# Performance work log

Measured on AMD Instinct MI355X. Metric: run time of the kernel, lower is better.

## Reference

```python
import jax, jax.numpy as jnp
import numpy as np
from jax import lax

# --- COSMO-SAC constants (defaults from the layer) ---
T = 623.15
Q0 = 79.53
R0 = 66.69
C_HB = 85580.0
RGAS = 8.3144598 / 4184.0
SIG_HB = 0.0084
EPS = 3.667
AEFF = 7.5
EO = 0.0002395
ZC = 10.0
X0 = 0.235
X1 = 1.0 - 0.235
N_SIGMA = 51
N_ITERS = 50


def _deltaw():
    s = np.linspace(-0.025, 0.025, N_SIGMA)
    sigma_m = np.tile(s, (N_SIGMA, 1))          # rows of grid values
    sigma_n = sigma_m.T
    sigma_acc = np.tril(sigma_n) + np.triu(sigma_m, 1)
    sigma_don = np.tril(sigma_m) + np.triu(sigma_n, 1)
    fpol = (EPS - 1.0) / (EPS + 0.5)
    alpha = 0.3 * AEFF ** 1.5 / EO
    alpha_prime = fpol * alpha
    dw = (alpha_prime / 2.0 * (sigma_m + sigma_n) ** 2
          + C_HB * np.maximum(0.0, sigma_acc - SIG_HB) * np.minimum(0.0, sigma_don + SIG_HB))
    return jnp.asarray(dw, jnp.float32)

DELTAW = _deltaw()                       # [51,51]
SSS = jnp.exp(-DELTAW / (RGAS * T))      # [51,51]


def get_Gamma(psigma):
    """50-step fixed-point solve. psigma: [B,51] -> Gamma: [B,51]."""
    AA = SSS[None, :, :] * psigma[:, None, :]   # [B,51,51]
    def step(G, _):
        Gnew = 1.0 / jnp.einsum('bmn,bn->bm', AA, G)
        return (Gnew + G) * 0.5, None
    G, _ = lax.scan(step, jnp.ones_like(psigma), None, length=N_ITERS)
    return G


def setup_inputs() -> dict:
    key = jax.random.key(0)
    k1, k2, k3, k4 = jax.random.split(key, 4)
    B = 32768
    return {
        "input_my_sigma": jax.random.uniform(k1, (B, N_SIGMA), dtype=jnp.float32),
        "v_compound": jax.random.uniform(k2, (B,), dtype=jnp.float32),
        "input_vt_sigma": jax.random.uniform(k3, (B, N_SIGMA, 2), dtype=jnp.float32),
        "v_vt": jax.random.uniform(k4, (B,), dtype=jnp.float32),
    }


def reference(input_my_sigma, v_compound, input_vt_sigma, v_vt):
    my = input_my_sigma                 # [B,51]
    vt = input_vt_sigma[:, :, 1]        # [B,51]
    A0 = jnp.sum(my, axis=1)            # [B]
    A1 = jnp.sum(vt, axis=1)            # [B]

    psigma_mix = (X0 * my + X1 * vt) / (X0 * A0[:, None] + X1 * A1[:, None])
    lnGamma_mix = jnp.log(get_Gamma(psigma_mix))       # [B,51]

    # residual part for component i = 0
    psigma = my / A0[:, None]
    lnGammai = jnp.log(get_Gamma(psigma))              # [B,51]
    lng_resid = A0 / AEFF * jnp.sum(psigma * (lnGamma_mix - lnGammai), axis=1)

    # combinatorial part (Staverman-Guggenheim)
    q0 = A0 / Q0
    q1 = A1 / Q0
    r0 = v_compound / R0
    r1 = v_vt / R0
    xq = X0 * q0 + X1 * q1
    xr = X0 * r0 + X1 * r1
    theta = X0 * q0 / xq
    phi = X0 * r0 / xr
    l0 = ZC / 2.0 * (r0 - q0) - (r0 - 1.0)
    l1 = ZC / 2.0 * (r1 - q1) - (r1 - 1.0)
    xl = X0 * l0 + X1 * l1
    lng_comb = (jnp.log(phi / X0) + ZC / 2.0 * q0 * jnp.log(theta / phi)
                + l0 - phi / X0 * xl)

    return (lng_resid + lng_comb)[:, None]             # [B,1]
```

## Files before the change

kernel.cpp:

```cpp
#include <hip/hip_runtime.h>

typedef __bf16 bf16;
typedef __attribute__((ext_vector_type(4))) bf16 bf16x4;
typedef __attribute__((ext_vector_type(8))) bf16 bf16x8;
typedef __attribute__((ext_vector_type(4))) float f32x4;

namespace {

constexpr double csqrt(double x) {
  double s = x > 1 ? x : 1;
  for (int i = 0; i < 60; ++i) s = 0.5 * (s + x / s);
  return s;
}
constexpr double AP_D =
    ((3.667 - 1.0) / (3.667 + 0.5)) * (0.3 * (7.5 * csqrt(7.5)) / 0.0002395);
constexpr double RGAST_D = (8.3144598 / 4184.0) * 623.15;

__device__ __forceinline__ float sss_val(int i, int j) {
  if (i > 50 || j > 50) return 0.0f;
  const float si = -0.025f + 0.001f * (float)i;
  const float sj = -0.025f + 0.001f * (float)j;
  const float acc = fmaxf(0.0f, fmaxf(si, sj) - 0.0084f);
  const float don = fminf(0.0f, fminf(si, sj) + 0.0084f);
  const float dw = (float)(AP_D * 0.5) * (si + sj) * (si + sj) + 85580.0f * acc * don;
  return expf(-dw * (float)(1.0 / RGAST_D));
}

__device__ __forceinline__ float fast_log(float x) {
  return __builtin_amdgcn_logf(x) * 0.69314718056f;
}

__device__ __forceinline__ f32x4 mfma16(bf16x8 a, bf16x8 b, f32x4 c) {
  return __builtin_amdgcn_mfma_f32_16x16x32_bf16(a, b, c, 0, 0, 0);
}

}

__global__ __launch_bounds__(64, 4) void cosmo_mfma_gt(
    const float* __restrict__ my_sigma,
    const float* __restrict__ v_comp,
    const float* __restrict__ vt_sigma,
    const float* __restrict__ v_vt,
    float* __restrict__ out,
    int B)
{
  __shared__ bf16 lds[16 * 68];

  const int lane = threadIdx.x;
  const int s    = lane & 15;
  const int g    = lane >> 4;
  const int e    = blockIdx.x * 8 + (s >> 1);
  const int task = s & 1;
  const bool ein = (e < B);
  const int  ec  = ein ? e : 0;

  float A0, A1, wC[16];
  {
    float myv[16], vtv[16];
#pragma unroll
    for (int t = 0; t < 4; ++t)
#pragma unroll
      for (int r = 0; r < 4; ++r) {
        const int n  = 16 * t + 4 * g + r;
        const bool nv = (n < 51) && ein;
        const int nc = (n < 51) ? n : 50;
        myv[4 * t + r] = nv ? my_sigma[(size_t)ec * 51 + nc] : 0.0f;
        vtv[4 * t + r] = nv ? vt_sigma[((size_t)ec * 51 + nc) * 2 + 1] : 0.0f;
      }
    float pA0 = 0.f, pA1 = 0.f;
#pragma unroll
    for (int i = 0; i < 16; ++i) { pA0 += myv[i]; pA1 += vtv[i]; }
    A0 = pA0; A0 += __shfl_xor(A0, 16, 64); A0 += __shfl_xor(A0, 32, 64);
    A1 = pA1; A1 += __shfl_xor(A1, 16, 64); A1 += __shfl_xor(A1, 32, 64);

    const float den  = task ? (0.235f * A0 + 0.765f * A1) : A0;
    const float rden = __builtin_amdgcn_rcpf(den);
#pragma unroll
    for (int i = 0; i < 16; ++i) {
      const float num = task ? (0.235f * myv[i] + 0.765f * vtv[i]) : myv[i];
      wC[i] = num * rden;
    }
  }

  float Gt[16];
#pragma unroll
  for (int i = 0; i < 16; ++i) Gt[i] = wC[i];

  bf16x8 afr[4][2];
#pragma unroll
  for (int t = 0; t < 4; ++t)
#pragma unroll
    for (int kt = 0; kt < 2; ++kt) {
      bf16x8 v;
#pragma unroll
      for (int i = 0; i < 8; ++i)
        v[i] = (bf16)sss_val(16 * t + s, 32 * kt + 8 * g + i);
      afr[t][kt] = v;
    }

  const int wb = s * 68 + 4 * g;
  const int rb = s * 68 + 8 * g;
  float padd[4];
#pragma unroll
  for (int r = 0; r < 4; ++r) padd[r] = (4 * g + r >= 3) ? 1.0f : 0.0f;

#pragma unroll 1
  for (int it = 0; it < 50; ++it) {
#pragma unroll
    for (int t = 0; t < 4; ++t) {
      bf16x4 hv;
#pragma unroll
      for (int r = 0; r < 4; ++r) hv[r] = (bf16)Gt[4 * t + r];
      *(bf16x4*)(lds + wb + 16 * t) = hv;
    }

    bf16x8 bfr[2];
#pragma unroll
    for (int kt = 0; kt < 2; ++kt) {
      const bf16x4 lo = *(const bf16x4*)(lds + rb + 32 * kt);
      const bf16x4 hi = *(const bf16x4*)(lds + rb + 32 * kt + 4);
      bfr[kt] = __builtin_shufflevector(lo, hi, 0, 1, 2, 3, 4, 5, 6, 7);
    }

    const f32x4 z = {};
    f32x4 acc[4];
#pragma unroll
    for (int t = 0; t < 4; ++t) acc[t] = mfma16(afr[t][0], bfr[0], z);
#pragma unroll
    for (int t = 0; t < 4; ++t) acc[t] = mfma16(afr[t][1], bfr[1], acc[t]);

#pragma unroll
    for (int t = 0; t < 3; ++t)
#pragma unroll
      for (int r = 0; r < 4; ++r) {
        const int i = 4 * t + r;
        const float rc = __builtin_amdgcn_rcpf(acc[t][r]);
        Gt[i] = 0.5f * __builtin_fmaf(wC[i], rc, Gt[i]);
      }
#pragma unroll
    for (int r = 0; r < 4; ++r) {
      const int i = 12 + r;
      const float rc = __builtin_amdgcn_rcpf(acc[3][r] + padd[r]);
      Gt[i] = 0.5f * __builtin_fmaf(wC[i], rc, Gt[i]);
    }
  }

  const float rA0 = __builtin_amdgcn_rcpf(A0);
  float Sp = 0.f;
#pragma unroll
  for (int t = 0; t < 4; ++t)
#pragma unroll
    for (int r = 0; r < 4; ++r) {
      const int n = 16 * t + 4 * g + r;
      if (n < 51) {
        const int i = 4 * t + r;
        const float p  = (ein ? my_sigma[(size_t)ec * 51 + n] : 0.0f) * rA0;
        const float gg = Gt[i] * __builtin_amdgcn_rcpf(wC[i]);
        Sp += p * __builtin_amdgcn_logf(gg);
      }
    }
  Sp += __shfl_xor(Sp, 16, 64);
  Sp += __shfl_xor(Sp, 32, 64);
  const float St = Sp * 0.69314718056f;
  const float So = __shfl_xor(St, 1, 64);

  if (task == 0 && g == 0 && ein) {
    const float lng_resid = A0 * (1.0f / 7.5f) * (So - St);
    const float v0  = v_comp[e];
    const float v1v = v_vt[e];
    const float q0 = A0 * (1.0f / 79.53f), q1 = A1 * (1.0f / 79.53f);
    const float r0 = v0 * (1.0f / 66.69f), r1 = v1v * (1.0f / 66.69f);
    const float xq = 0.235f * q0 + 0.765f * q1;
    const float xr = 0.235f * r0 + 0.765f * r1;
    const float theta = 0.235f * q0 * __builtin_amdgcn_rcpf(xq);
    const float phi   = 0.235f * r0 * __builtin_amdgcn_rcpf(xr);
    const float l0 = 5.0f * (r0 - q0) - (r0 - 1.0f);
    const float l1 = 5.0f * (r1 - q1) - (r1 - 1.0f);
    const float xl = 0.235f * l0 + 0.765f * l1;
    const float lng_comb = fast_log(phi * (1.0f / 0.235f))
                         + 5.0f * q0 * fast_log(theta * __builtin_amdgcn_rcpf(phi))
                         + l0 - (phi * (1.0f / 0.235f)) * xl;
    out[e] = lng_resid + lng_comb;
  }
}

extern "C" void kernel_launch(void* const* d_in, const int* in_sizes, int n_in,
                              void* d_out, int out_size, void* d_ws, size_t ws_size,
                              hipStream_t stream) {
  const float* my  = (const float*)d_in[0];
  const float* vc  = (const float*)d_in[1];
  const float* vts = (const float*)d_in[2];
  const float* vvt = (const float*)d_in[3];
  float* out = (float*)d_out;
  const int B = in_sizes[1];
  const int grid = (B + 7) / 8;
  cosmo_mfma_gt<<<grid, 64, 0, stream>>>(my, vc, vts, vvt, out, B);
}
```

Baseline: 122.6 us.

## Permute SSS K-ordering to feed MFMA B operand from registers, drop LDS

The SSS A-fragment columns are reordered so the K index each lane contributes matches the accumulator rows it already holds. The updated Gamma values can then go straight from registers into the B operand, with no per-iteration LDS write/read round trip. Blocks also grow from one to four wavefronts, each handling eight batch elements, so fewer blocks are launched. A guard against zero wC is added in the final log, which avoids a divide-by-zero on padded entries.

```diff
diff --git a/kernel.cpp b/kernel.cpp
--- a/kernel.cpp
+++ b/kernel.cpp
@@ -36,7 +36,7 @@
 
 }
 
-__global__ __launch_bounds__(64, 4) void cosmo_mfma_gt(
+__global__ __launch_bounds__(256, 4) void cosmo_mfma_perm(
     const float* __restrict__ my_sigma,
     const float* __restrict__ v_comp,
     const float* __restrict__ vt_sigma,
@@ -44,12 +44,11 @@
     float* __restrict__ out,
     int B)
 {
-  __shared__ bf16 lds[16 * 68];
-
-  const int lane = threadIdx.x;
+  const int lane = threadIdx.x & 63;
+  const int wv   = threadIdx.x >> 6;
   const int s    = lane & 15;
   const int g    = lane >> 4;
-  const int e    = blockIdx.x * 8 + (s >> 1);
+  const int e    = blockIdx.x * 32 + wv * 8 + (s >> 1);
   const int task = s & 1;
   const bool ein = (e < B);
   const int  ec  = ein ? e : 0;
@@ -88,53 +87,46 @@
 
   bf16x8 afr[4][2];
 #pragma unroll
-  for (int t = 0; t < 4; ++t)
+  for (int tp = 0; tp < 4; ++tp)
 #pragma unroll
     for (int kt = 0; kt < 2; ++kt) {
       bf16x8 v;
 #pragma unroll
-      for (int i = 0; i < 8; ++i)
-        v[i] = (bf16)sss_val(16 * t + s, 32 * kt + 8 * g + i);
-      afr[t][kt] = v;
+      for (int i = 0; i < 8; ++i) {
+        const int n_src = 16 * (2 * kt + (i >> 2)) + 4 * g + (i & 3);
+        v[i] = (bf16)sss_val(16 * tp + s, n_src);
+      }
+      afr[tp][kt] = v;
     }
 
-  const int wb = s * 68 + 4 * g;
-  const int rb = s * 68 + 8 * g;
   float padd[4];
 #pragma unroll
   for (int r = 0; r < 4; ++r) padd[r] = (4 * g + r >= 3) ? 1.0f : 0.0f;
 
 #pragma unroll 1
   for (int it = 0; it < 50; ++it) {
+    bf16x4 hb[4];
 #pragma unroll
-    for (int t = 0; t < 4; ++t) {
-      bf16x4 hv;
+    for (int t = 0; t < 4; ++t)
 #pragma unroll
-      for (int r = 0; r < 4; ++r) hv[r] = (bf16)Gt[4 * t + r];
-      *(bf16x4*)(lds + wb + 16 * t) = hv;
-    }
+      for (int r = 0; r < 4; ++r) hb[t][r] = (bf16)Gt[4 * t + r];
 
-    bf16x8 bfr[2];
-#pragma unroll
-    for (int kt = 0; kt < 2; ++kt) {
-      const bf16x4 lo = *(const bf16x4*)(lds + rb + 32 * kt);
-      const bf16x4 hi = *(const bf16x4*)(lds + rb + 32 * kt + 4);
-      bfr[kt] = __builtin_shufflevector(lo, hi, 0, 1, 2, 3, 4, 5, 6, 7);
-    }
+    const bf16x8 b0 = __builtin_shufflevector(hb[0], hb[1], 0, 1, 2, 3, 4, 5, 6, 7);
+    const bf16x8 b1 = __builtin_shufflevector(hb[2], hb[3], 0, 1, 2, 3, 4, 5, 6, 7);
 
     const f32x4 z = {};
     f32x4 acc[4];
 #pragma unroll
-    for (int t = 0; t < 4; ++t) acc[t] = mfma16(afr[t][0], bfr[0], z);
+    for (int tp = 0; tp < 4; ++tp) acc[tp] = mfma16(afr[tp][0], b0, z);
 #pragma unroll
-    for (int t = 0; t < 4; ++t) acc[t] = mfma16(afr[t][1], bfr[1], acc[t]);
+    for (int tp = 0; tp < 4; ++tp) acc[tp] = mfma16(afr[tp][1], b1, acc[tp]);
 
 #pragma unroll
-    for (int t = 0; t < 3; ++t)
+    for (int tp = 0; tp < 3; ++tp)
 #pragma unroll
       for (int r = 0; r < 4; ++r) {
-        const int i = 4 * t + r;
-        const float rc = __builtin_amdgcn_rcpf(acc[t][r]);
+        const int i = 4 * tp + r;
+        const float rc = __builtin_amdgcn_rcpf(acc[tp][r]);
         Gt[i] = 0.5f * __builtin_fmaf(wC[i], rc, Gt[i]);
       }
 #pragma unroll
@@ -155,7 +147,8 @@
       if (n < 51) {
         const int i = 4 * t + r;
         const float p  = (ein ? my_sigma[(size_t)ec * 51 + n] : 0.0f) * rA0;
-        const float gg = Gt[i] * __builtin_amdgcn_rcpf(wC[i]);
+        const float gg = (wC[i] != 0.0f)
+                           ? Gt[i] * __builtin_amdgcn_rcpf(wC[i]) : 1.0f;
         Sp += p * __builtin_amdgcn_logf(gg);
       }
     }
@@ -193,6 +186,6 @@
   const float* vvt = (const float*)d_in[3];
   float* out = (float*)d_out;
   const int B = in_sizes[1];
-  const int grid = (B + 7) / 8;
-  cosmo_mfma_gt<<<grid, 64, 0, stream>>>(my, vc, vts, vvt, out, B);
+  const int grid = (B + 31) / 32;
+  cosmo_mfma_perm<<<grid, 256, 0, stream>>>(my, vc, vts, vvt, out, B);
 }
```

Result: faster. 115.7 us (-5.6%).
